# Kernel tuning notes

Measured on AMD Instinct MI355X. Metric: run time of the kernel, lower is better.

Reference implementation:

```python
import jax, jax.numpy as jnp
import numpy as np
import math

N_HEADS = 8
TANH_CLIP = 10.0
TEMP = 1.0


def setup_inputs() -> dict:
    key = jax.random.key(0)
    ks = jax.random.split(key, 8)
    B, N, D = 256, 2048, 128
    node_embeddings = jax.random.normal(ks[0], (B, N, D), dtype=jnp.float32)
    W_node = jax.random.normal(ks[1], (D, 3 * D), dtype=jnp.float32) / math.sqrt(D)
    W_fixed = jax.random.normal(ks[2], (D, D), dtype=jnp.float32) / math.sqrt(D)
    W_step = jax.random.normal(ks[3], (2 * D, D), dtype=jnp.float32) / math.sqrt(2 * D)
    W_out = jax.random.normal(ks[4], (D, D), dtype=jnp.float32) / math.sqrt(D)
    first_idx = jax.random.randint(ks[5], (B,), 0, N, dtype=jnp.int32)
    last_idx = jax.random.randint(ks[6], (B,), 0, N, dtype=jnp.int32)
    mask = jax.random.bernoulli(ks[7], 0.5, (B, N))
    mask = mask.at[:, 0].set(False)  # guarantee at least one feasible node per row
    return {"node_embeddings": node_embeddings, "W_node": W_node, "W_fixed": W_fixed,
            "W_step": W_step, "W_out": W_out, "first_idx": first_idx,
            "last_idx": last_idx, "mask": mask}


def reference(node_embeddings, W_node, W_fixed, W_step, W_out, first_idx, last_idx, mask):
    B, N, D = node_embeddings.shape
    H = N_HEADS
    hd = D // H  # key_dim = val_dim = embed_dim / n_heads
    neg_inf = -jnp.inf

    # --- _precompute ---
    graph_embed = node_embeddings.mean(axis=1)                # [B, D]
    fixed_context = graph_embed @ W_fixed                     # [B, D]
    proj = node_embeddings @ W_node                           # [B, N, 3D]
    gK, gV, logit_K = jnp.split(proj, 3, axis=-1)             # each [B, N, D]
    gK = gK.reshape(B, N, H, hd).transpose(2, 0, 1, 3)        # [H, B, N, hd]
    gV = gV.reshape(B, N, H, hd).transpose(2, 0, 1, 3)        # [H, B, N, hd]

    # --- step context: cat(first node emb, last node emb) ---
    first_emb = jnp.take_along_axis(node_embeddings, first_idx[:, None, None].astype(jnp.int32), axis=1)[:, 0]  # [B, D]
    last_emb = jnp.take_along_axis(node_embeddings, last_idx[:, None, None].astype(jnp.int32), axis=1)[:, 0]
    step_ctx = jnp.concatenate([first_emb, last_emb], axis=-1)  # [B, 2D]
    query = fixed_context + step_ctx @ W_step                 # [B, D]

    # --- glimpse multi-head attention (n_query = 1, masked inner) ---
    Q = query.reshape(B, H, hd).transpose(1, 0, 2)            # [H, B, hd]
    compat = jnp.einsum('hbd,hbnd->hbn', Q, gK) / math.sqrt(hd)  # [H, B, N]
    compat = jnp.where(mask[None, :, :], neg_inf, compat)     # mask_inner=True
    attn = jax.nn.softmax(compat, axis=-1)
    heads = jnp.einsum('hbn,hbnd->hbd', attn, gV)             # [H, B, hd]
    glimpse = heads.transpose(1, 0, 2).reshape(B, D) @ W_out  # project_out, [B, D]

    # --- logits with tanh clipping and masking ---
    logits = jnp.einsum('bd,bnd->bn', glimpse, logit_K) / math.sqrt(D)  # [B, N]
    logits = jnp.tanh(logits) * TANH_CLIP
    logits = jnp.where(mask, neg_inf, logits)                 # mask_logits=True
    log_p = jax.nn.log_softmax(logits / TEMP, axis=-1)        # [B, N]
    return log_p
```

## Files before the change

### kernel.cpp

```cpp
#include <hip/hip_runtime.h>
#include <math.h>

#define B_ 256
#define N_ 2048
#define D_ 128

#define NEG_HUGE (-1.0e30f)

#define WSA_STRIDE 1040
#define WSA_SIZE (B_ * 8 * WSA_STRIDE)
#define WSB_OFF WSA_SIZE
#define WSB_SIZE (B_ * 8 * 2)
#define WSC_OFF (WSB_OFF + WSB_SIZE)

typedef __attribute__((ext_vector_type(8))) short bf16x8;
typedef __attribute__((ext_vector_type(4))) float f32x4;
typedef __attribute__((ext_vector_type(4))) unsigned short u16x4;

__device__ __forceinline__ float wave_max64(float v) {
#pragma unroll
  for (int off = 32; off > 0; off >>= 1) v = fmaxf(v, __shfl_xor(v, off, 64));
  return v;
}
__device__ __forceinline__ float wave_sum64(float v) {
#pragma unroll
  for (int off = 32; off > 0; off >>= 1) v += __shfl_xor(v, off, 64);
  return v;
}
__device__ __forceinline__ unsigned short bf16rne(float f) {
  unsigned u = __float_as_uint(f);
  u += 0x7FFFu + ((u >> 16) & 1u);
  return (unsigned short)(u >> 16);
}

__global__ void __launch_bounds__(128) k_partial(const float* __restrict__ emb,
                                                 float* __restrict__ buf) {
  const int b = blockIdx.x, s = blockIdx.y;
  const int t = threadIdx.x;
  const int f4 = t & 31, ng = t >> 5;
  const float4* base = (const float4*)(emb + (size_t)b * N_ * D_);
  float4 acc = make_float4(0.f, 0.f, 0.f, 0.f);
  int n = s * 256 + ng;
#pragma unroll 4
  for (int i = 0; i < 64; ++i, n += 4) {
    float4 v = base[(size_t)n * 32 + f4];
    acc.x += v.x; acc.y += v.y; acc.z += v.z; acc.w += v.w;
  }
  __shared__ float4 red[128];
  red[t] = acc;
  __syncthreads();
  if (ng == 0) {
    float4 a = red[f4], bb = red[32 + f4], c = red[64 + f4], d = red[96 + f4];
    float4 r = make_float4(a.x + bb.x + c.x + d.x, a.y + bb.y + c.y + d.y,
                           a.z + bb.z + c.z + d.z, a.w + bb.w + c.w + d.w);
    *((float4*)(buf + (size_t)b * N_ + s * 128) + f4) = r;
  }
}

__global__ void __launch_bounds__(128) k_query(const float* __restrict__ emb,
                                               const float* __restrict__ Wfix,
                                               const float* __restrict__ Wstep,
                                               const float* __restrict__ Wnode,
                                               const int* __restrict__ fidx,
                                               const int* __restrict__ lidx,
                                               float* __restrict__ buf) {
  const int b = blockIdx.x, t = threadIdx.x;
  __shared__ float ge[128], fe[128], le[128], q[128];
  float s = 0.f;
  const float* part = buf + (size_t)b * N_;
#pragma unroll
  for (int i = 0; i < 8; ++i) s += part[i * 128 + t];
  ge[t] = s * (1.0f / 2048.0f);
  const int fi = fidx[b], li = lidx[b];
  fe[t] = emb[(size_t)b * N_ * D_ + (size_t)fi * D_ + t];
  le[t] = emb[(size_t)b * N_ * D_ + (size_t)li * D_ + t];
  __syncthreads();
  float acc = 0.f;
  for (int k = 0; k < 128; ++k) acc = fmaf(ge[k], Wfix[k * 128 + t], acc);
  for (int k = 0; k < 128; ++k) acc = fmaf(fe[k], Wstep[k * 128 + t], acc);
  for (int k = 0; k < 128; ++k) acc = fmaf(le[k], Wstep[(128 + k) * 128 + t], acc);
  q[t] = acc;
  __syncthreads();
  const float* wrow = Wnode + (size_t)t * 384;
#pragma unroll
  for (int h = 0; h < 8; ++h) {
    float a = 0.f;
#pragma unroll
    for (int k = 0; k < 16; ++k) a = fmaf(q[h * 16 + k], wrow[h * 16 + k], a);
    buf[(size_t)b * N_ + 1024 + h * 128 + t] = a * 0.25f;
  }
}

__global__ void __launch_bounds__(256) k_attn_m(const float* __restrict__ emb,
                                                const unsigned char* __restrict__ mask,
                                                const float* __restrict__ buf,
                                                float* __restrict__ wsA) {
  const int b = blockIdx.x, s = blockIdx.y, t = threadIdx.x;
  const int lane = t & 63, w = t >> 6;
  const int lg = lane >> 4, lc = lane & 15;

  __shared__ __align__(16) unsigned short eR[64][136];
  __shared__ __align__(16) unsigned short eC[128][72];
  __shared__ __align__(16) unsigned short pT[16][72];
  __shared__ float red0[4][16];
  __shared__ float red1[4][16];
  __shared__ float resc_s[16];
  __shared__ unsigned char mask_s[64];

  bf16x8 bq[4];
#pragma unroll
  for (int ks = 0; ks < 4; ++ks)
#pragma unroll
    for (int j = 0; j < 8; ++j) bq[ks][j] = 0;
  if (lc < 8) {
    const float* qrow = buf + (size_t)b * N_ + 1024 + lc * 128;
#pragma unroll
    for (int ks = 0; ks < 4; ++ks)
#pragma unroll
      for (int j = 0; j < 8; ++j)
        bq[ks][j] = (short)bf16rne(qrow[32 * ks + 8 * lg + j]);
  }

  float m_run = -INFINITY, l_run = 0.f;
  f32x4 wacc0 = {0.f, 0.f, 0.f, 0.f}, wacc1 = {0.f, 0.f, 0.f, 0.f};
  const float* embb = emb + ((size_t)b * N_ + s * 256) * D_;
  const unsigned char* mrow = mask + (size_t)b * N_ + s * 256;

  for (int tile = 0; tile < 4; ++tile) {
    {
      const float* src = embb + (size_t)tile * 64 * D_;
#pragma unroll
      for (int i = 0; i < 4; ++i) {
        const int gid = t + 256 * i;
        const int n = gid >> 4, d0 = (gid & 15) * 8;
        const float4 v0 = *(const float4*)(src + (size_t)n * D_ + d0);
        const float4 v1 = *(const float4*)(src + (size_t)n * D_ + d0 + 4);
        bf16x8 ev;
        ev[0] = (short)bf16rne(v0.x); ev[1] = (short)bf16rne(v0.y);
        ev[2] = (short)bf16rne(v0.z); ev[3] = (short)bf16rne(v0.w);
        ev[4] = (short)bf16rne(v1.x); ev[5] = (short)bf16rne(v1.y);
        ev[6] = (short)bf16rne(v1.z); ev[7] = (short)bf16rne(v1.w);
        *(bf16x8*)&eR[n][d0] = ev;
      }
      if (t < 64) mask_s[t] = mrow[tile * 64 + t];
    }
    __syncthreads();

    {
      const int d = t >> 1, n0 = (t & 1) * 32;
#pragma unroll
      for (int jb = 0; jb < 4; ++jb) {
        bf16x8 cv;
#pragma unroll
        for (int i = 0; i < 8; ++i) cv[i] = (short)eR[n0 + 8 * jb + i][d];
        *(bf16x8*)&eC[d][n0 + 8 * jb] = cv;
      }
    }

    f32x4 sAcc = {0.f, 0.f, 0.f, 0.f};
#pragma unroll
    for (int ks = 0; ks < 4; ++ks) {
      const bf16x8 af = *(const bf16x8*)&eR[16 * w + lc][32 * ks + 8 * lg];
      sAcc = __builtin_amdgcn_mfma_f32_16x16x32_bf16(af, bq[ks], sAcc, 0, 0, 0);
    }

    float sv[4];
    bool mk[4];
    float tmax = -INFINITY;
#pragma unroll
    for (int r = 0; r < 4; ++r) {
      mk[r] = mask_s[16 * w + 4 * lg + r] != 0;
      sv[r] = mk[r] ? -INFINITY : sAcc[r];
      tmax = fmaxf(tmax, sv[r]);
    }
    tmax = fmaxf(tmax, __shfl_xor(tmax, 16, 64));
    tmax = fmaxf(tmax, __shfl_xor(tmax, 32, 64));
    if (lane < 16) red0[w][lc] = tmax;
    __syncthreads();

    const float m_tile = fmaxf(fmaxf(red0[0][lc], red0[1][lc]),
                               fmaxf(red0[2][lc], red0[3][lc]));
    const float m_new = fmaxf(m_run, m_tile);
    const float rsc = (m_new == -INFINITY) ? 1.f : __expf(m_run - m_new);
    float psum = 0.f;
    unsigned short pu[4];
#pragma unroll
    for (int r = 0; r < 4; ++r) {
      const float p = mk[r] ? 0.f : __expf(sv[r] - m_new);
      psum += p;
      pu[r] = bf16rne(p);
    }
    m_run = m_new;
    psum += __shfl_xor(psum, 16, 64);
    psum += __shfl_xor(psum, 32, 64);
    if (lane < 16) red1[w][lc] = psum;
    *(u16x4*)&pT[lc][16 * w + 4 * lg] = (u16x4){pu[0], pu[1], pu[2], pu[3]};
    if (t < 16) resc_s[t] = rsc;
    __syncthreads();

    l_run = l_run * rsc + (red1[0][lc] + red1[1][lc] + red1[2][lc] + red1[3][lc]);

    {
      const float r0f = resc_s[4 * lg + 0], r1f = resc_s[4 * lg + 1];
      const float r2f = resc_s[4 * lg + 2], r3f = resc_s[4 * lg + 3];
      wacc0[0] *= r0f; wacc0[1] *= r1f; wacc0[2] *= r2f; wacc0[3] *= r3f;
      wacc1[0] *= r0f; wacc1[1] *= r1f; wacc1[2] *= r2f; wacc1[3] *= r3f;
    }
#pragma unroll
    for (int ks = 0; ks < 2; ++ks) {
      const bf16x8 pa = *(const bf16x8*)&pT[lc][32 * ks + 8 * lg];
      const bf16x8 b0 = *(const bf16x8*)&eC[16 * w + lc][32 * ks + 8 * lg];
      const bf16x8 b1 = *(const bf16x8*)&eC[16 * (w + 4) + lc][32 * ks + 8 * lg];
      wacc0 = __builtin_amdgcn_mfma_f32_16x16x32_bf16(pa, b0, wacc0, 0, 0, 0);
      wacc1 = __builtin_amdgcn_mfma_f32_16x16x32_bf16(pa, b1, wacc1, 0, 0, 0);
    }
    __syncthreads();
  }

  float* dst = wsA + (size_t)(b * 8 + s) * WSA_STRIDE;
  if (lg < 2) {
#pragma unroll
    for (int r = 0; r < 4; ++r) {
      const int h = 4 * lg + r;
      dst[16 + h * 128 + 16 * w + lc] = wacc0[r];
      dst[16 + h * 128 + 16 * (w + 4) + lc] = wacc1[r];
    }
  }
  if (t < 8) { dst[t] = m_run; dst[8 + t] = l_run; }
}

__global__ void __launch_bounds__(128) k_attn_comb(const float* __restrict__ Wnode,
                                                   const float* __restrict__ Wout,
                                                   const float* __restrict__ wsA,
                                                   float* __restrict__ wsC) {
  const int b = blockIdx.x, t = threadIdx.x;
  const float* base = wsA + (size_t)b * 8 * WSA_STRIDE;
  __shared__ float Ls[8], scale[8][8];
  __shared__ float wl[8 * 128], heads[128], glim[128];

  if (t < 8) {
    float M = -INFINITY;
#pragma unroll
    for (int s = 0; s < 8; ++s) M = fmaxf(M, base[s * WSA_STRIDE + t]);
    float L = 0.f;
#pragma unroll
    for (int s = 0; s < 8; ++s) {
      const float m = base[s * WSA_STRIDE + t];
      const float sc = (m == -INFINITY) ? 0.f : expf(m - M);
      scale[s][t] = sc;
      L = fmaf(base[s * WSA_STRIDE + 8 + t], sc, L);
    }
    Ls[t] = L;
  }
  __syncthreads();
#pragma unroll
  for (int h = 0; h < 8; ++h) {
    float acc = 0.f;
#pragma unroll
    for (int s = 0; s < 8; ++s)
      acc = fmaf(scale[s][h], base[s * WSA_STRIDE + 16 + h * 128 + t], acc);
    wl[h * 128 + t] = acc;
  }
  __syncthreads();
  {
    const int h = t >> 4, k = t & 15;
    float hv = 0.f;
    const float* wp = Wnode + 128 + h * 16 + k;
    for (int d = 0; d < 128; ++d) hv = fmaf(wl[h * 128 + d], wp[(size_t)d * 384], hv);
    heads[t] = hv / Ls[h];
  }
  __syncthreads();
  {
    float g = 0.f;
    for (int j = 0; j < 128; ++j) g = fmaf(heads[j], Wout[j * 128 + t], g);
    glim[t] = g;
  }
  __syncthreads();
  {
    float cv = 0.f;
    const float* wr = Wnode + (size_t)t * 384 + 256;
    for (int j = 0; j < 128; ++j) cv = fmaf(wr[j], glim[j], cv);
    wsC[(size_t)b * 128 + t] = cv * 0.08838834764831845f;
  }
}

__global__ void __launch_bounds__(256) k_logits_part(const float* __restrict__ emb,
                                                     const unsigned char* __restrict__ mask,
                                                     const float* __restrict__ wsC,
                                                     float* __restrict__ buf,
                                                     float* __restrict__ wsB) {
  const int b = blockIdx.x, s = blockIdx.y;
  const int t = threadIdx.x, lane = t & 63, w = t >> 6;
  __shared__ __align__(16) float emb_lds[64][132];
  __shared__ float part[4][64];
  const float* embb = emb + (size_t)b * N_ * D_;
  const unsigned char* mrow = mask + (size_t)b * N_;

  float4 cq[8];
  {
    const float4* c4 = (const float4*)(wsC + (size_t)b * 128);
#pragma unroll
    for (int j = 0; j < 8; ++j) cq[j] = c4[w * 8 + j];
  }
  float mr = NEG_HUGE, sr = 0.f;
  for (int tile = 0; tile < 4; ++tile) {
    const int n0 = s * 256 + tile * 64;
    int gid = t;
#pragma unroll
    for (int i = 0; i < 8; ++i, gid += 256) {
      int r = gid >> 5, c4i = gid & 31;
      *(float4*)&emb_lds[r][c4i * 4] =
          *(const float4*)(embb + (size_t)(n0 + r) * D_ + c4i * 4);
    }
    __syncthreads();
    const float* er = &emb_lds[lane][w * 32];
    float acc = 0.f;
#pragma unroll
    for (int j = 0; j < 8; ++j) {
      float4 e = *(const float4*)(er + 4 * j);
      acc = fmaf(e.x, cq[j].x, fmaf(e.y, cq[j].y, fmaf(e.z, cq[j].z, fmaf(e.w, cq[j].w, acc))));
    }
    part[w][lane] = acc;
    __syncthreads();
    const float v = part[0][lane] + part[1][lane] + part[2][lane] + part[3][lane];
    const bool msk = mrow[n0 + lane] != 0;
    const float val = msk ? NEG_HUGE : 10.f * tanhf(v);
    const float tm = wave_max64(val);
    const float mn = fmaxf(mr, tm);
    sr = sr * expf(mr - mn) + wave_sum64(msk ? 0.f : expf(val - mn));
    mr = mn;
    if (w == 0) buf[(size_t)b * N_ + n0 + lane] = val;
    __syncthreads();
  }
  if (t == 0) {
    wsB[(size_t)(b * 8 + s) * 2] = mr;
    wsB[(size_t)(b * 8 + s) * 2 + 1] = sr;
  }
}

__global__ void __launch_bounds__(256) k_norm(const float* __restrict__ wsB,
                                              float* __restrict__ buf) {
  const int b = blockIdx.x, t = threadIdx.x;
  __shared__ float LSs;
  if (t == 0) {
    float M = NEG_HUGE;
#pragma unroll
    for (int q = 0; q < 8; ++q) M = fmaxf(M, wsB[(size_t)(b * 8 + q) * 2]);
    float S = 0.f;
#pragma unroll
    for (int q = 0; q < 8; ++q) {
      const float m = wsB[(size_t)(b * 8 + q) * 2];
      S += wsB[(size_t)(b * 8 + q) * 2 + 1] * expf(m - M);
    }
    LSs = M + logf(S);
  }
  __syncthreads();
  const float LS = LSs;
#pragma unroll
  for (int i = 0; i < 8; ++i) {
    const size_t idx = (size_t)b * N_ + t + 256 * i;
    const float v = buf[idx];
    buf[idx] = (v <= -1.0e29f) ? NEG_HUGE : (v - LS);
  }
}

extern "C" void kernel_launch(void* const* d_in, const int* in_sizes, int n_in,
                              void* d_out, int out_size, void* d_ws, size_t ws_size,
                              hipStream_t stream) {
  (void)in_sizes; (void)n_in; (void)out_size; (void)ws_size;
  const float* emb = (const float*)d_in[0];
  const float* Wnode = (const float*)d_in[1];
  const float* Wfix = (const float*)d_in[2];
  const float* Wstep = (const float*)d_in[3];
  const float* Wout = (const float*)d_in[4];
  const int* fidx = (const int*)d_in[5];
  const int* lidx = (const int*)d_in[6];
  const unsigned char* mask = (const unsigned char*)d_in[7];
  float* buf = (float*)d_out;
  float* ws = (float*)d_ws;

  k_partial<<<dim3(B_, 8), 128, 0, stream>>>(emb, buf);
  k_query<<<B_, 128, 0, stream>>>(emb, Wfix, Wstep, Wnode, fidx, lidx, buf);
  k_attn_m<<<dim3(B_, 8), 256, 0, stream>>>(emb, mask, buf, ws);
  k_attn_comb<<<B_, 128, 0, stream>>>(Wnode, Wout, ws, ws + WSC_OFF);
  k_logits_part<<<dim3(B_, 8), 256, 0, stream>>>(emb, mask, ws + WSC_OFF, buf, ws + WSB_OFF);
  k_norm<<<B_, 256, 0, stream>>>(ws + WSB_OFF, buf);
}
```

Before: 171.6 us.

## Use transposing LDS reads for attention and shuffle-reduce logits without LDS staging

The attention kernel stores bf16 embeddings in a blocked LDS layout and reads the transposed V operand with ds_read_b64_tr_b16. This removes the explicit eC transpose pass and its LDS buffer. The logits kernel now computes dot products directly from global loads with wave shuffles instead of staging through LDS, and replaces tanhf and expf with fast exp-based forms. The risks are the inline asm layout being hard to verify, small accuracy changes from the fast math, and more shuffle instructions per loaded element.

```diff
diff --git a/kernel.cpp b/kernel.cpp
--- a/kernel.cpp
+++ b/kernel.cpp
@@ -16,6 +16,7 @@
 typedef __attribute__((ext_vector_type(8))) short bf16x8;
 typedef __attribute__((ext_vector_type(4))) float f32x4;
 typedef __attribute__((ext_vector_type(4))) unsigned short u16x4;
+typedef __attribute__((ext_vector_type(2))) int i32x2;
 
 __device__ __forceinline__ float wave_max64(float v) {
 #pragma unroll
@@ -99,9 +100,8 @@
   const int lane = t & 63, w = t >> 6;
   const int lg = lane >> 4, lc = lane & 15;
 
-  __shared__ __align__(16) unsigned short eR[64][136];
-  __shared__ __align__(16) unsigned short eC[128][72];
-  __shared__ __align__(16) unsigned short pT[16][72];
+  __shared__ __align__(16) unsigned short eR[9216];
+  __shared__ __align__(16) unsigned short pT[16 * 72];
   __shared__ float red0[4][16];
   __shared__ float red1[4][16];
   __shared__ float resc_s[16];
@@ -140,27 +140,19 @@
         ev[2] = (short)bf16rne(v0.z); ev[3] = (short)bf16rne(v0.w);
         ev[4] = (short)bf16rne(v1.x); ev[5] = (short)bf16rne(v1.y);
         ev[6] = (short)bf16rne(v1.z); ev[7] = (short)bf16rne(v1.w);
-        *(bf16x8*)&eR[n][d0] = ev;
+        const int widx = ((n >> 2) * 8 + (d0 >> 4)) * 72 + ((n & 3) << 4) + (d0 & 15);
+        *(bf16x8*)&eR[widx] = ev;
       }
       if (t < 64) mask_s[t] = mrow[tile * 64 + t];
     }
     __syncthreads();
 
-    {
-      const int d = t >> 1, n0 = (t & 1) * 32;
-#pragma unroll
-      for (int jb = 0; jb < 4; ++jb) {
-        bf16x8 cv;
-#pragma unroll
-        for (int i = 0; i < 8; ++i) cv[i] = (short)eR[n0 + 8 * jb + i][d];
-        *(bf16x8*)&eC[d][n0 + 8 * jb] = cv;
-      }
-    }
-
     f32x4 sAcc = {0.f, 0.f, 0.f, 0.f};
 #pragma unroll
     for (int ks = 0; ks < 4; ++ks) {
-      const bf16x8 af = *(const bf16x8*)&eR[16 * w + lc][32 * ks + 8 * lg];
+      const int aidx = ((4 * w + (lc >> 2)) * 8 + 2 * ks + (lg >> 1)) * 72 +
+                       ((lc & 3) << 4) + ((lg & 1) << 3);
+      const bf16x8 af = *(const bf16x8*)&eR[aidx];
       sAcc = __builtin_amdgcn_mfma_f32_16x16x32_bf16(af, bq[ks], sAcc, 0, 0, 0);
     }
 
@@ -194,7 +186,7 @@
     psum += __shfl_xor(psum, 16, 64);
     psum += __shfl_xor(psum, 32, 64);
     if (lane < 16) red1[w][lc] = psum;
-    *(u16x4*)&pT[lc][16 * w + 4 * lg] = (u16x4){pu[0], pu[1], pu[2], pu[3]};
+    *(u16x4*)&pT[lc * 72 + 16 * w + 4 * lg] = (u16x4){pu[0], pu[1], pu[2], pu[3]};
     if (t < 16) resc_s[t] = rsc;
     __syncthreads();
 
@@ -206,13 +198,44 @@
       wacc0[0] *= r0f; wacc0[1] *= r1f; wacc0[2] *= r2f; wacc0[3] *= r3f;
       wacc1[0] *= r0f; wacc1[1] *= r1f; wacc1[2] *= r2f; wacc1[3] *= r3f;
     }
-#pragma unroll
-    for (int ks = 0; ks < 2; ++ks) {
-      const bf16x8 pa = *(const bf16x8*)&pT[lc][32 * ks + 8 * lg];
-      const bf16x8 b0 = *(const bf16x8*)&eC[16 * w + lc][32 * ks + 8 * lg];
-      const bf16x8 b1 = *(const bf16x8*)&eC[16 * (w + 4) + lc][32 * ks + 8 * lg];
-      wacc0 = __builtin_amdgcn_mfma_f32_16x16x32_bf16(pa, b0, wacc0, 0, 0, 0);
-      wacc1 = __builtin_amdgcn_mfma_f32_16x16x32_bf16(pa, b1, wacc1, 0, 0, 0);
+
+    i32x2 tb0a, tb0b, tb1a, tb1b, tb2a, tb2b, tb3a, tb3b;
+    {
+      const unsigned base00 = (unsigned)(unsigned long long)
+          &eR[((0 + 2 * lg) * 8 + w) * 72 + lc];
+      const unsigned base01 = (unsigned)(unsigned long long)
+          &eR[((0 + 2 * lg) * 8 + (w + 4)) * 72 + lc];
+      const unsigned base10 = (unsigned)(unsigned long long)
+          &eR[((8 + 2 * lg) * 8 + w) * 72 + lc];
+      const unsigned base11 = (unsigned)(unsigned long long)
+          &eR[((8 + 2 * lg) * 8 + (w + 4)) * 72 + lc];
+      asm volatile("ds_read_b64_tr_b16 %0, %2 offset:0\n\t"
+                   "ds_read_b64_tr_b16 %1, %2 offset:1152"
+                   : "=v"(tb0a), "=v"(tb0b) : "v"(base00));
+      asm volatile("ds_read_b64_tr_b16 %0, %2 offset:0\n\t"
+                   "ds_read_b64_tr_b16 %1, %2 offset:1152"
+                   : "=v"(tb1a), "=v"(tb1b) : "v"(base01));
+      asm volatile("ds_read_b64_tr_b16 %0, %2 offset:0\n\t"
+                   "ds_read_b64_tr_b16 %1, %2 offset:1152"
+                   : "=v"(tb2a), "=v"(tb2b) : "v"(base10));
+      asm volatile("ds_read_b64_tr_b16 %0, %2 offset:0\n\t"
+                   "ds_read_b64_tr_b16 %1, %2 offset:1152"
+                   : "=v"(tb3a), "=v"(tb3b) : "v"(base11));
+      asm volatile("s_waitcnt lgkmcnt(0)" ::: "memory");
+      __builtin_amdgcn_sched_barrier(0);
+    }
+    {
+      const bf16x8 pa0 = *(const bf16x8*)&pT[lc * 72 + 8 * lg];
+      const bf16x8 pa1 = *(const bf16x8*)&pT[lc * 72 + 32 + 8 * lg];
+      union { i32x2 d[2]; bf16x8 v; } u;
+      u.d[0] = tb0a; u.d[1] = tb0b;
+      wacc0 = __builtin_amdgcn_mfma_f32_16x16x32_bf16(pa0, u.v, wacc0, 0, 0, 0);
+      u.d[0] = tb1a; u.d[1] = tb1b;
+      wacc1 = __builtin_amdgcn_mfma_f32_16x16x32_bf16(pa0, u.v, wacc1, 0, 0, 0);
+      u.d[0] = tb2a; u.d[1] = tb2b;
+      wacc0 = __builtin_amdgcn_mfma_f32_16x16x32_bf16(pa1, u.v, wacc0, 0, 0, 0);
+      u.d[0] = tb3a; u.d[1] = tb3b;
+      wacc1 = __builtin_amdgcn_mfma_f32_16x16x32_bf16(pa1, u.v, wacc1, 0, 0, 0);
     }
     __syncthreads();
   }
@@ -291,45 +314,38 @@
                                                      float* __restrict__ wsB) {
   const int b = blockIdx.x, s = blockIdx.y;
   const int t = threadIdx.x, lane = t & 63, w = t >> 6;
-  __shared__ __align__(16) float emb_lds[64][132];
-  __shared__ float part[4][64];
-  const float* embb = emb + (size_t)b * N_ * D_;
-  const unsigned char* mrow = mask + (size_t)b * N_;
-
-  float4 cq[8];
-  {
-    const float4* c4 = (const float4*)(wsC + (size_t)b * 128);
-#pragma unroll
-    for (int j = 0; j < 8; ++j) cq[j] = c4[w * 8 + j];
-  }
+  __shared__ float lg[64];
+  const float4 cf = ((const float4*)(wsC + (size_t)b * 128))[t & 31];
+  const float* embb = emb + ((size_t)b * N_ + s * 256) * D_;
+  const unsigned char* mrow = mask + (size_t)b * N_ + s * 256;
   float mr = NEG_HUGE, sr = 0.f;
+
   for (int tile = 0; tile < 4; ++tile) {
-    const int n0 = s * 256 + tile * 64;
-    int gid = t;
-#pragma unroll
-    for (int i = 0; i < 8; ++i, gid += 256) {
-      int r = gid >> 5, c4i = gid & 31;
-      *(float4*)&emb_lds[r][c4i * 4] =
-          *(const float4*)(embb + (size_t)(n0 + r) * D_ + c4i * 4);
-    }
-    __syncthreads();
-    const float* er = &emb_lds[lane][w * 32];
-    float acc = 0.f;
-#pragma unroll
-    for (int j = 0; j < 8; ++j) {
-      float4 e = *(const float4*)(er + 4 * j);
-      acc = fmaf(e.x, cq[j].x, fmaf(e.y, cq[j].y, fmaf(e.z, cq[j].z, fmaf(e.w, cq[j].w, acc))));
-    }
-    part[w][lane] = acc;
-    __syncthreads();
-    const float v = part[0][lane] + part[1][lane] + part[2][lane] + part[3][lane];
-    const bool msk = mrow[n0 + lane] != 0;
-    const float val = msk ? NEG_HUGE : 10.f * tanhf(v);
+    const int n0 = tile * 64;
+#pragma unroll
+    for (int i = 0; i < 8; ++i) {
+      const int gid = t + 256 * i;
+      const int r = gid >> 5, c = (gid & 31) * 4;
+      const float4 e = *(const float4*)(embb + (size_t)(n0 + r) * D_ + c);
+      float p = fmaf(e.x, cf.x, fmaf(e.y, cf.y, fmaf(e.z, cf.z, e.w * cf.w)));
+      p += __shfl_xor(p, 16, 64);
+      p += __shfl_xor(p, 8, 64);
+      p += __shfl_xor(p, 4, 64);
+      p += __shfl_xor(p, 2, 64);
+      p += __shfl_xor(p, 1, 64);
+      if ((t & 31) == 0) lg[r] = p;
+    }
+    __syncthreads();
+
+    const bool mk = mrow[n0 + lane] != 0;
+    const float x = lg[lane];
+    const float ex = __expf(2.f * x);
+    const float val = mk ? NEG_HUGE : (10.f - __fdividef(20.f, ex + 1.f));
     const float tm = wave_max64(val);
     const float mn = fmaxf(mr, tm);
-    sr = sr * expf(mr - mn) + wave_sum64(msk ? 0.f : expf(val - mn));
+    sr = sr * __expf(mr - mn) + wave_sum64(mk ? 0.f : __expf(val - mn));
     mr = mn;
-    if (w == 0) buf[(size_t)b * N_ + n0 + lane] = val;
+    if (w == 0) buf[(size_t)b * N_ + s * 256 + n0 + lane] = val;
     __syncthreads();
   }
   if (t == 0) {
```

After: 167.6 us. 1.02x faster.
